# Optimization experiments

Hardware: AMD Instinct MI355X
Metric: run time of the kernel (lower is better)

Reference implementation:

```python
import jax, jax.numpy as jnp
import numpy as np

S, B, M, F, C = 32, 128, 128, 512, 100


def setup_inputs() -> dict:
    key = jax.random.key(0)
    k = jax.random.split(key, 7)
    x = jax.random.normal(k[0], (B, F), dtype=jnp.float32)
    y = jax.random.randint(k[1], (B,), 0, C, dtype=jnp.int32)
    # Z in {-1, +1}: Bernoulli(0.5) sample mapped via 2*b - 1 (mirrors sample_Z)
    Zb = (jax.random.uniform(k[2], (S, B, M)) < 0.5).astype(jnp.float32)
    Z = 2.0 * Zb - 1.0
    alpha_0 = jax.random.normal(k[3], (M,), dtype=jnp.float32)
    init_c = 2.0 / np.sqrt(F)
    alpha = init_c * jax.random.normal(k[4], (M, F), dtype=jnp.float32)
    alpha = alpha / jnp.linalg.norm(alpha, axis=0, keepdims=True)
    beta_0 = jax.random.normal(k[5], (C,), dtype=jnp.float32)
    init_c2 = 2.0 / np.sqrt(M)
    beta = init_c2 * jax.random.normal(k[6], (C, M), dtype=jnp.float32)
    return {"x": x, "y": y, "Z": Z, "alpha_0": alpha_0, "alpha": alpha,
            "beta_0": beta_0, "beta": beta}


def reference(x, y, Z, alpha_0, alpha, beta_0, beta):
    # linear_eta / eta (compute_linear_eta, compute_eta)
    linear_eta = alpha_0[None, :] + x @ alpha.T            # [B, M]
    eta = jax.nn.sigmoid(linear_eta)                        # exp(l)/(1+exp(l))

    y_onehot = jax.nn.one_hot(y, C, dtype=Z.dtype)          # [B, C]
    # Unperturbed logits shared across all j (rank-1 structure of compute_pi_j)
    base = beta_0[None, None, :] + jnp.einsum('sbm,cm->sbc', Z, beta)  # [S,B,C]

    def pi_for(target):
        # Flipping column j of Z to `target` shifts logits by (target - Z_j)*beta[:, j]
        delta = (target - Z)[..., None] * beta.T[None, None, :, :]  # [S,B,M,C]
        lin = base[:, :, None, :] + delta                            # [S,B,M,C]
        # NOTE: original ADDS the max (faithful to source); softmax ratio unchanged
        lin = lin + jnp.max(lin, axis=-1, keepdims=True)
        num = jnp.sum(y_onehot[None, :, None, :] * lin, axis=-1)     # [S,B,M]
        den = jnp.sum(jnp.exp(lin), axis=-1)                         # [S,B,M]
        return jnp.exp(num) / den                                    # [S,B,M]

    pi_pos = pi_for(1.0)
    pi_neg = pi_for(-1.0)
    # compute_EY_X_j: sum over Monte-Carlo samples
    EY_X_j = jnp.sum(pi_pos * eta[None] + pi_neg * (1.0 - eta)[None], axis=0)  # [B,M]
    return EY_X_j
```

## Files before the change

### kernel.cpp

```cpp
#include <hip/hip_runtime.h>
#include <math.h>

#define S_ 32
#define B_ 128
#define M_ 128
#define F_ 512
#define C_ 100
#define SB 8

typedef _Float16 f16;
typedef _Float16 f16x8 __attribute__((ext_vector_type(8)));
typedef float f32x4 __attribute__((ext_vector_type(4)));

#define WS_BT  0
#define WS_EP  28672
#define WS_EN  61440
#define WS_ETA 94208

__global__ __launch_bounds__(512) void k_pre(
    const float* __restrict__ x, const float* __restrict__ alpha0,
    const float* __restrict__ alpha, const float* __restrict__ beta,
    char* __restrict__ ws, float* __restrict__ out) {
  const int bid = blockIdx.x;
  const int tid = threadIdx.x;
  __shared__ float betaS[C_ * M_];
  if (bid < 256) {
    const int b = bid >> 1, mh = bid & 1;
    float* etag = (float*)(ws + WS_ETA);
    const int lane = tid & 63, w = tid >> 6, l15 = lane & 15, lg = lane >> 4;
    if (tid < 64) out[b * M_ + mh * 64 + tid] = 0.f;
    const float4* x4 = (const float4*)x;
    const float4* a4 = (const float4*)alpha;
    float4 xr[8];
#pragma unroll
    for (int r = 0; r < 8; ++r) xr[r] = x4[b * 128 + r * 16 + l15];
#pragma unroll
    for (int j = 0; j < 2; ++j) {
      int m = mh * 64 + w * 8 + j * 4 + lg;
      float acc = 0.f;
#pragma unroll
      for (int r = 0; r < 8; ++r) {
        float4 av = a4[(size_t)m * 128 + r * 16 + l15];
        float4 xv = xr[r];
        acc = fmaf(av.x, xv.x, acc); acc = fmaf(av.y, xv.y, acc);
        acc = fmaf(av.z, xv.z, acc); acc = fmaf(av.w, xv.w, acc);
      }
      acc += __shfl_xor(acc, 1);
      acc += __shfl_xor(acc, 2);
      acc += __shfl_xor(acc, 4);
      acc += __shfl_xor(acc, 8);
      if (l15 == 0) {
        float l = alpha0[m] + acc;
        etag[b * 128 + m] = 1.f / (1.f + __expf(-l));
      }
    }
  } else {
    for (int i = tid; i < C_ * M_; i += 512) betaS[i] = beta[i];
    __syncthreads();
    const int ci = (bid - 256) * 512 + tid;
    if (ci < 1792) {
      int lane = ci & 63, t = ci >> 6;
      int ct = t % 7, kc = t / 7;
      int c = ct * 16 + (lane & 15);
      int m0 = kc * 32 + (lane >> 4) * 8;
      f16x8 v;
#pragma unroll
      for (int i = 0; i < 8; ++i)
        v[i] = (c < C_) ? (f16)betaS[c * M_ + m0 + i] : (f16)0.f;
      *(f16x8*)(ws + WS_BT + (size_t)ci * 16) = v;
    } else if (ci < 3840) {
      int q = ci - 1792;
      int lane = q & 63, t = q >> 6;
      int m = (t & 7) * 16 + (lane & 15);
      int c0 = (t >> 3) * 32 + (lane >> 4) * 8;
      f16x8 v;
#pragma unroll
      for (int i = 0; i < 8; ++i) {
        int c = c0 + i;
        v[i] = (c < C_) ? (f16)__expf(2.f * betaS[c * M_ + m]) : (f16)0.f;
      }
      *(f16x8*)(ws + WS_EP + (size_t)q * 16) = v;
    } else if (ci < 5888) {
      int q = ci - 3840;
      int lane = q & 63, t = q >> 6;
      int m = (t & 7) * 16 + (lane & 15);
      int c0 = (t >> 3) * 32 + (lane >> 4) * 8;
      f16x8 v;
#pragma unroll
      for (int i = 0; i < 8; ++i) {
        int c = c0 + i;
        v[i] = (c < C_) ? (f16)__expf(-2.f * betaS[c * M_ + m]) : (f16)0.f;
      }
      *(f16x8*)(ws + WS_EN + (size_t)q * 16) = v;
    }
  }
}

__global__ __launch_bounds__(512) void k_main(
    const int* __restrict__ y, const float* __restrict__ Z,
    const float* __restrict__ beta0, const float* __restrict__ beta,
    const char* __restrict__ ws, float* __restrict__ out) {
  const int sh = blockIdx.x;
  const int b = blockIdx.y;
  const int tid = threadIdx.x;
  const int lane = tid & 63;
  const int w = tid >> 6;
  const int l15 = lane & 15;
  const int lg = lane >> 4;
  const int s0 = sh * SB;

  __shared__ __align__(16) f16 ZAf[256 * 8];
  __shared__ __align__(16) f16 PtAf[256 * 8];
  __shared__ float baseS[SB * 112];
  __shared__ float PybS[SB];

  const int yb = y[b];
  const int m = w * 16 + l15;

  if (tid < 256) {
    int s = tid;
    int kcs = s >> 6, lgs = (s >> 4) & 3, l15s = s & 15;
    f16x8 hv = {0, 0, 0, 0, 0, 0, 0, 0};
    if (l15s < SB) {
      const float* zrow = Z + ((size_t)(s0 + l15s) * B_ + b) * M_ + kcs * 32 + lgs * 8;
      float4 u0 = *(const float4*)zrow;
      float4 u1 = *(const float4*)(zrow + 4);
      hv = (f16x8){(f16)u0.x, (f16)u0.y, (f16)u0.z, (f16)u0.w,
                   (f16)u1.x, (f16)u1.y, (f16)u1.z, (f16)u1.w};
    }
    *(f16x8*)&ZAf[s * 8] = hv;
  }

  f16x8 bfr[4], bp[4], bn[4];
#pragma unroll
  for (int kc = 0; kc < 4; ++kc) {
    bp[kc] = *(const f16x8*)(ws + WS_EP + (size_t)((kc * 8 + w) * 64 + lane) * 16);
    bn[kc] = *(const f16x8*)(ws + WS_EN + (size_t)((kc * 8 + w) * 64 + lane) * 16);
    bfr[kc] = *(const f16x8*)(ws + WS_BT + (size_t)((kc * 7 + (w % 7)) * 64 + lane) * 16);
  }
  const float bym = beta[yb * M_ + m];
  const float eta_v = ((const float*)(ws + WS_ETA))[b * M_ + m];

  __syncthreads();

  if (w < 7) {
    f32x4 acc = {0.f, 0.f, 0.f, 0.f};
#pragma unroll
    for (int kc = 0; kc < 4; ++kc) {
      f16x8 a0 = *(const f16x8*)&ZAf[(kc * 64 + lane) * 8];
      acc = __builtin_amdgcn_mfma_f32_16x16x32_f16(a0, bfr[kc], acc, 0, 0, 0);
    }
    int col = w * 16 + l15;
    float b0v = (col < C_) ? beta0[col] : 0.f;
    if (lg < 2) {
#pragma unroll
      for (int j = 0; j < 4; ++j) baseS[(lg * 4 + j) * 112 + col] = acc[j] + b0v;
    }
  }
  __syncthreads();

  {
    int p = w;
    float v1 = baseS[p * 112 + lane];
    float v2 = (lane < 36) ? baseS[p * 112 + 64 + lane] : -1e30f;
    float mx = fmaxf(v1, v2);
#pragma unroll
    for (int off = 32; off > 0; off >>= 1) mx = fmaxf(mx, __shfl_xor(mx, off));
    float e1 = __expf(v1 - mx);
    float e2 = (lane < 36) ? __expf(v2 - mx) : 0.f;
    float sm = e1 + e2;
#pragma unroll
    for (int off = 32; off > 0; off >>= 1) sm += __shfl_xor(sm, off);
    float rd = 1.f / sm;
    float p1 = e1 * rd;
    float p2 = (lane < 36) ? e2 * rd : 0.f;
    {
      int c = lane, kc = c >> 5, lg2 = (c >> 3) & 3, ii = c & 7;
      PtAf[(kc * 64 + lg2 * 16 + p) * 8 + ii] = (f16)p1;
      PtAf[(kc * 64 + lg2 * 16 + p + 8) * 8 + ii] = (f16)0.f;
    }
    {
      int c = lane + 64, kc = c >> 5, lg2 = (c >> 3) & 3, ii = c & 7;
      PtAf[(kc * 64 + lg2 * 16 + p) * 8 + ii] = (f16)p2;
      PtAf[(kc * 64 + lg2 * 16 + p + 8) * 8 + ii] = (f16)0.f;
    }
    if (lane == yb) PybS[p] = p1;
    if (lane + 64 == yb) PybS[p] = p2;
  }
  __syncthreads();

  {
    f32x4 pA = {0.f, 0.f, 0.f, 0.f}, nA = {0.f, 0.f, 0.f, 0.f};
#pragma unroll
    for (int kc = 0; kc < 4; ++kc) {
      f16x8 a0 = *(const f16x8*)&PtAf[(kc * 64 + lane) * 8];
      pA = __builtin_amdgcn_mfma_f32_16x16x32_f16(a0, bp[kc], pA, 0, 0, 0);
      nA = __builtin_amdgcn_mfma_f32_16x16x32_f16(a0, bn[kc], nA, 0, 0, 0);
    }
    float epy = __expf(2.f * bym), eny = 1.f / epy;
    float ome = 1.f - eta_v;
    float o = 0.f;
    int kcz = m >> 5, lgz = (m >> 3) & 3, iiz = m & 7;
    if (lg < 2) {
#pragma unroll
      for (int j = 0; j < 4; ++j) {
        int p = lg * 4 + j;
        float z = (float)ZAf[(kcz * 64 + lgz * 16 + p) * 8 + iiz];
        float pyb = PybS[p];
        o += (z > 0.f) ? fmaf(pyb, eta_v, (pyb * eny / nA[j]) * ome)
                       : fmaf(pyb * epy / pA[j], eta_v, pyb * ome);
      }
    }
    o += __shfl_xor(o, 16);
    o += __shfl_xor(o, 32);
    if (lane < 16) atomicAdd(&out[b * M_ + w * 16 + l15], o);
  }
}

extern "C" void kernel_launch(void* const* d_in, const int* in_sizes, int n_in,
                              void* d_out, int out_size, void* d_ws, size_t ws_size,
                              hipStream_t stream) {
  const float* x = (const float*)d_in[0];
  const int* y = (const int*)d_in[1];
  const float* Z = (const float*)d_in[2];
  const float* alpha0 = (const float*)d_in[3];
  const float* alpha = (const float*)d_in[4];
  const float* beta0 = (const float*)d_in[5];
  const float* beta = (const float*)d_in[6];
  float* out = (float*)d_out;
  char* ws = (char*)d_ws;

  k_pre<<<dim3(268), dim3(512), 0, stream>>>(x, alpha0, alpha, beta, ws, out);
  k_main<<<dim3(4, B_), dim3(512), 0, stream>>>(y, Z, beta0, beta, ws, out);
}
```

Before: 15.47 us.

## Fill all 16 MFMA rows with samples, halving main grid and pre blocks

The main kernel now processes 16 Monte-Carlo samples per block instead of 8, so the 16-row MFMA tiles carry no zero padding and the grid drops to 2x128 blocks. Each wave handles two softmax rows, and the padding writes and lg<2 guards are removed. The eta prologue also computes all 128 m per block, so it uses 128 blocks instead of 256. The result is fewer blocks with more per-block serial work, which lowers parallelism on a device with many CUs.

Result: faster. 14.43 us (-6.7%).

```diff
diff --git a/kernel.cpp b/kernel.cpp
--- a/kernel.cpp
+++ b/kernel.cpp
@@ -6,7 +6,7 @@
 #define M_ 128
 #define F_ 512
 #define C_ 100
-#define SB 8
+#define SB 16
 
 typedef _Float16 f16;
 typedef _Float16 f16x8 __attribute__((ext_vector_type(8)));
@@ -24,19 +24,18 @@
   const int bid = blockIdx.x;
   const int tid = threadIdx.x;
   __shared__ float betaS[C_ * M_];
-  if (bid < 256) {
-    const int b = bid >> 1, mh = bid & 1;
+  if (bid < B_) {
     float* etag = (float*)(ws + WS_ETA);
     const int lane = tid & 63, w = tid >> 6, l15 = lane & 15, lg = lane >> 4;
-    if (tid < 64) out[b * M_ + mh * 64 + tid] = 0.f;
+    if (tid < M_) out[bid * M_ + tid] = 0.f;
     const float4* x4 = (const float4*)x;
     const float4* a4 = (const float4*)alpha;
     float4 xr[8];
 #pragma unroll
-    for (int r = 0; r < 8; ++r) xr[r] = x4[b * 128 + r * 16 + l15];
-#pragma unroll
-    for (int j = 0; j < 2; ++j) {
-      int m = mh * 64 + w * 8 + j * 4 + lg;
+    for (int r = 0; r < 8; ++r) xr[r] = x4[bid * 128 + r * 16 + l15];
+#pragma unroll
+    for (int j = 0; j < 4; ++j) {
+      int m = w * 16 + j * 4 + lg;
       float acc = 0.f;
 #pragma unroll
       for (int r = 0; r < 8; ++r) {
@@ -51,13 +50,13 @@
       acc += __shfl_xor(acc, 8);
       if (l15 == 0) {
         float l = alpha0[m] + acc;
-        etag[b * 128 + m] = 1.f / (1.f + __expf(-l));
+        etag[bid * 128 + m] = 1.f / (1.f + __expf(-l));
       }
     }
   } else {
     for (int i = tid; i < C_ * M_; i += 512) betaS[i] = beta[i];
     __syncthreads();
-    const int ci = (bid - 256) * 512 + tid;
+    const int ci = (bid - B_) * 512 + tid;
     if (ci < 1792) {
       int lane = ci & 63, t = ci >> 6;
       int ct = t % 7, kc = t / 7;
@@ -107,7 +106,6 @@
   const int w = tid >> 6;
   const int l15 = lane & 15;
   const int lg = lane >> 4;
-  const int s0 = sh * SB;
 
   __shared__ __align__(16) f16 ZAf[256 * 8];
   __shared__ __align__(16) f16 PtAf[256 * 8];
@@ -119,15 +117,13 @@
 
   if (tid < 256) {
     int s = tid;
-    int kcs = s >> 6, lgs = (s >> 4) & 3, l15s = s & 15;
-    f16x8 hv = {0, 0, 0, 0, 0, 0, 0, 0};
-    if (l15s < SB) {
-      const float* zrow = Z + ((size_t)(s0 + l15s) * B_ + b) * M_ + kcs * 32 + lgs * 8;
-      float4 u0 = *(const float4*)zrow;
-      float4 u1 = *(const float4*)(zrow + 4);
-      hv = (f16x8){(f16)u0.x, (f16)u0.y, (f16)u0.z, (f16)u0.w,
-                   (f16)u1.x, (f16)u1.y, (f16)u1.z, (f16)u1.w};
-    }
+    int kcs = s >> 6, lgs = (s >> 4) & 3, p = s & 15;
+    const float* zrow =
+        Z + ((size_t)(sh * SB + p) * B_ + b) * M_ + kcs * 32 + lgs * 8;
+    float4 u0 = *(const float4*)zrow;
+    float4 u1 = *(const float4*)(zrow + 4);
+    f16x8 hv = {(f16)u0.x, (f16)u0.y, (f16)u0.z, (f16)u0.w,
+                (f16)u1.x, (f16)u1.y, (f16)u1.z, (f16)u1.w};
     *(f16x8*)&ZAf[s * 8] = hv;
   }
 
@@ -140,6 +136,8 @@
   }
   const float bym = beta[yb * M_ + m];
   const float eta_v = ((const float*)(ws + WS_ETA))[b * M_ + m];
+  const int colB = w * 16 + l15;
+  const float b0v = (w < 7 && colB < C_) ? beta0[colB] : 0.f;
 
   __syncthreads();
 
@@ -150,42 +148,39 @@
       f16x8 a0 = *(const f16x8*)&ZAf[(kc * 64 + lane) * 8];
       acc = __builtin_amdgcn_mfma_f32_16x16x32_f16(a0, bfr[kc], acc, 0, 0, 0);
     }
-    int col = w * 16 + l15;
-    float b0v = (col < C_) ? beta0[col] : 0.f;
-    if (lg < 2) {
-#pragma unroll
-      for (int j = 0; j < 4; ++j) baseS[(lg * 4 + j) * 112 + col] = acc[j] + b0v;
-    }
+#pragma unroll
+    for (int j = 0; j < 4; ++j) baseS[(lg * 4 + j) * 112 + colB] = acc[j] + b0v;
   }
   __syncthreads();
 
   {
-    int p = w;
-    float v1 = baseS[p * 112 + lane];
-    float v2 = (lane < 36) ? baseS[p * 112 + 64 + lane] : -1e30f;
-    float mx = fmaxf(v1, v2);
-#pragma unroll
-    for (int off = 32; off > 0; off >>= 1) mx = fmaxf(mx, __shfl_xor(mx, off));
-    float e1 = __expf(v1 - mx);
-    float e2 = (lane < 36) ? __expf(v2 - mx) : 0.f;
-    float sm = e1 + e2;
-#pragma unroll
-    for (int off = 32; off > 0; off >>= 1) sm += __shfl_xor(sm, off);
-    float rd = 1.f / sm;
-    float p1 = e1 * rd;
-    float p2 = (lane < 36) ? e2 * rd : 0.f;
-    {
-      int c = lane, kc = c >> 5, lg2 = (c >> 3) & 3, ii = c & 7;
-      PtAf[(kc * 64 + lg2 * 16 + p) * 8 + ii] = (f16)p1;
-      PtAf[(kc * 64 + lg2 * 16 + p + 8) * 8 + ii] = (f16)0.f;
-    }
-    {
-      int c = lane + 64, kc = c >> 5, lg2 = (c >> 3) & 3, ii = c & 7;
-      PtAf[(kc * 64 + lg2 * 16 + p) * 8 + ii] = (f16)p2;
-      PtAf[(kc * 64 + lg2 * 16 + p + 8) * 8 + ii] = (f16)0.f;
-    }
-    if (lane == yb) PybS[p] = p1;
-    if (lane + 64 == yb) PybS[p] = p2;
+#pragma unroll
+    for (int k = 0; k < 2; ++k) {
+      int p = w * 2 + k;
+      float v1 = baseS[p * 112 + lane];
+      float v2 = (lane < 36) ? baseS[p * 112 + 64 + lane] : -1e30f;
+      float mx = fmaxf(v1, v2);
+#pragma unroll
+      for (int off = 32; off > 0; off >>= 1) mx = fmaxf(mx, __shfl_xor(mx, off));
+      float e1 = __expf(v1 - mx);
+      float e2 = (lane < 36) ? __expf(v2 - mx) : 0.f;
+      float sm = e1 + e2;
+#pragma unroll
+      for (int off = 32; off > 0; off >>= 1) sm += __shfl_xor(sm, off);
+      float rd = 1.f / sm;
+      float p1 = e1 * rd;
+      float p2 = (lane < 36) ? e2 * rd : 0.f;
+      {
+        int c = lane, kc = c >> 5, lg2 = (c >> 3) & 3, ii = c & 7;
+        PtAf[(kc * 64 + lg2 * 16 + p) * 8 + ii] = (f16)p1;
+      }
+      {
+        int c = lane + 64, kc = c >> 5, lg2 = (c >> 3) & 3, ii = c & 7;
+        PtAf[(kc * 64 + lg2 * 16 + p) * 8 + ii] = (f16)p2;
+      }
+      if (lane == yb) PybS[p] = p1;
+      if (lane + 64 == yb) PybS[p] = p2;
+    }
   }
   __syncthreads();
 
@@ -201,15 +196,13 @@
     float ome = 1.f - eta_v;
     float o = 0.f;
     int kcz = m >> 5, lgz = (m >> 3) & 3, iiz = m & 7;
-    if (lg < 2) {
-#pragma unroll
-      for (int j = 0; j < 4; ++j) {
-        int p = lg * 4 + j;
-        float z = (float)ZAf[(kcz * 64 + lgz * 16 + p) * 8 + iiz];
-        float pyb = PybS[p];
-        o += (z > 0.f) ? fmaf(pyb, eta_v, (pyb * eny / nA[j]) * ome)
-                       : fmaf(pyb * epy / pA[j], eta_v, pyb * ome);
-      }
+#pragma unroll
+    for (int j = 0; j < 4; ++j) {
+      int p = lg * 4 + j;
+      float z = (float)ZAf[(kcz * 64 + lgz * 16 + p) * 8 + iiz];
+      float pyb = PybS[p];
+      o += (z > 0.f) ? fmaf(pyb, eta_v, (pyb * eny / nA[j]) * ome)
+                     : fmaf(pyb * epy / pA[j], eta_v, pyb * ome);
     }
     o += __shfl_xor(o, 16);
     o += __shfl_xor(o, 32);
@@ -230,6 +223,6 @@
   float* out = (float*)d_out;
   char* ws = (char*)d_ws;
 
-  k_pre<<<dim3(268), dim3(512), 0, stream>>>(x, alpha0, alpha, beta, ws, out);
-  k_main<<<dim3(4, B_), dim3(512), 0, stream>>>(y, Z, beta0, beta, ws, out);
+  k_pre<<<dim3(B_ + 12), dim3(512), 0, stream>>>(x, alpha0, alpha, beta, ws, out);
+  k_main<<<dim3(2, B_), dim3(512), 0, stream>>>(y, Z, beta0, beta, ws, out);
 }
```
